# Kernel optimization log

Measured on AMD Instinct MI355X. Metric: run time of the kernel, lower is better.

Reference implementation:

```python
import jax, jax.numpy as jnp
import numpy as np

B, N, C, H = 8, 784, 768, 16
HEAD_DIM = C // H
SCALE = HEAD_DIM ** -0.5


def rel_indices(num_patches):
    # ConViT relative position features: (dx, dy, dx^2+dy^2) per patch pair
    s = int(num_patches ** 0.5)
    ind = (jnp.arange(s)[None, :] - jnp.arange(s)[:, None]).astype(jnp.float32)
    indx = jnp.tile(ind, (s, s))                               # [N, N]
    indy = jnp.repeat(jnp.repeat(ind, s, axis=0), s, axis=1)   # [N, N]
    indd = indx ** 2 + indy ** 2
    return jnp.stack([indx, indy, indd], axis=-1)              # [N, N, 3]


def setup_inputs() -> dict:
    key = jax.random.key(0)
    ks = jax.random.split(key, 6)
    std = 0.02
    return {
        "x": jax.random.normal(ks[0], (B, N, C), dtype=jnp.float32),
        "Wq": jax.random.normal(ks[1], (C, C), dtype=jnp.float32) * std,
        "Wk": jax.random.normal(ks[2], (C, C), dtype=jnp.float32) * std,
        "Wv": jax.random.normal(ks[3], (C, C), dtype=jnp.float32) * std,
        "Wproj": jax.random.normal(ks[4], (C, C), dtype=jnp.float32) * std,
        "b_proj": jnp.zeros((C,), dtype=jnp.float32),
        "W_pos": jax.random.normal(ks[5], (H, 3), dtype=jnp.float32) * std,
        "b_pos": jnp.zeros((H,), dtype=jnp.float32),
        "gating": jnp.ones((H,), dtype=jnp.float32),
    }


def reference(x, Wq, Wk, Wv, Wproj, b_proj, W_pos, b_pos, gating):
    b, n, c = x.shape
    h, d = H, c // H

    def heads(W):
        # torch Linear: y = x @ W.T ; reshape to [b, h, n, d]
        return (x @ W.T).reshape(b, n, h, d).transpose(0, 2, 1, 3)

    q, k, v = heads(Wq), heads(Wk), heads(Wv)

    # content score: [b, h, n, n]
    patch_score = jnp.einsum('bhnd,bhmd->bhnm', q, k) * SCALE
    patch_score = jax.nn.softmax(patch_score, axis=-1)

    # positional score: rel [n,n,3] -> [h,n,n], broadcast over batch
    rel = rel_indices(n)
    pos_score = jnp.einsum('nmc,hc->hnm', rel, W_pos) + b_pos[:, None, None]
    pos_score = jax.nn.softmax(pos_score, axis=-1)

    g = jax.nn.sigmoid(gating)[None, :, None, None]  # [1,h,1,1]
    attn = (1.0 - g) * patch_score + g * pos_score[None]
    attn = attn / jnp.sum(attn, axis=-1, keepdims=True)

    out = jnp.einsum('bhnm,bhmd->bhnd', attn, v)
    out = out.transpose(0, 2, 1, 3).reshape(b, n, c)
    out = out @ Wproj.T + b_proj
    return out, attn, v
```

## Files before the change

### kernel.cpp

```cpp
#include <hip/hip_runtime.h>
#include <math.h>

#define BB 8
#define NN 784
#define CC 768
#define HH 16
#define DD 48
#define SCALE 0.14433756729740643f

#define ATTN_OFF ((size_t)BB*NN*CC)
#define V_OFF (ATTN_OFF + (size_t)BB*HH*NN*NN)

#define WS_XB ((size_t)0)
#define WS_WB ((size_t)4816896)
#define WS_QB (WS_WB + (size_t)4*589824)
#define WS_KB (WS_QB + (size_t)4816896)
#define WS_VT (WS_KB + (size_t)4816896)
#define WS_OB (WS_VT + (size_t)4816896)

using bf16x8 = __attribute__((ext_vector_type(8))) short;
using f32x4  = __attribute__((ext_vector_type(4))) float;

__device__ __forceinline__ short f2bf(float f) {
    union { float f; unsigned u; } uf; uf.f = f;
    unsigned u = uf.u;
    return (short)((u + 0x7FFFu + ((u >> 16) & 1u)) >> 16);
}
__device__ __forceinline__ bf16x8 bzero() {
    bf16x8 z = {0,0,0,0,0,0,0,0};
    return z;
}
__device__ __forceinline__ bf16x8 cvt8v(f32x4 a, f32x4 b) {
    bf16x8 r;
    r[0]=f2bf(a[0]); r[1]=f2bf(a[1]); r[2]=f2bf(a[2]); r[3]=f2bf(a[3]);
    r[4]=f2bf(b[0]); r[5]=f2bf(b[1]); r[6]=f2bf(b[2]); r[7]=f2bf(b[3]);
    return r;
}
#define MFMA16(a,b,c) __builtin_amdgcn_mfma_f32_16x16x32_bf16((a),(b),(c),0,0,0)

__global__ __launch_bounds__(256) void cast_kernel(
    const float* __restrict__ x, const float* __restrict__ Wq,
    const float* __restrict__ Wk, const float* __restrict__ Wv,
    const float* __restrict__ Wp, short* __restrict__ xb, short* __restrict__ wb)
{
    int idx = blockIdx.x * 256 + threadIdx.x;
    const float* src;
    short* dst;
    if (idx < 1204224) {
        src = x + (size_t)idx * 4;
        dst = xb + (size_t)idx * 4;
    } else {
        int j = idx - 1204224;
        int sel = j / 147456;
        size_t off = (size_t)(j % 147456) * 4;
        const float* W = (sel == 0) ? Wq : (sel == 1) ? Wk : (sel == 2) ? Wv : Wp;
        src = W + off;
        dst = wb + (size_t)sel * 589824 + off;
    }
    f32x4 v = *(const f32x4*)src;
    union { short s[4]; uint2 u; } o;
    o.s[0] = f2bf(v[0]); o.s[1] = f2bf(v[1]); o.s[2] = f2bf(v[2]); o.s[3] = f2bf(v[3]);
    *(uint2*)dst = o.u;
}

__global__ __launch_bounds__(256) void qkv_mfma(
    const short* __restrict__ xb, const short* __restrict__ wb,
    short* __restrict__ qb, short* __restrict__ kb,
    float* __restrict__ vo, short* __restrict__ vt)
{
    const int t = threadIdx.x, l = t & 63, ww = t >> 6;
    const int quad = l >> 4, lc = l & 15;
    const int P = blockIdx.x, xcd = P & 7, ii = P >> 3;
    const int start = (xcd < 2) ? xcd * 111 : 222 + (xcd - 2) * 110;
    const int orig = start + ii;
    const int bx = orig / 18, bn = orig % 18;

    const int m0 = bx * 128 + (ww >> 1) * 64;
    const int wsel = bn / 6;
    const int colbase = (bn % 6) * 128 + (ww & 1) * 64;
    const short* W = wb + (size_t)wsel * 589824;

    f32x4 acc[4][4] = {};
    const short* arow = xb + (size_t)(m0 + lc) * 768 + quad * 8;
    const short* brow = W  + (size_t)(colbase + lc) * 768 + quad * 8;

    for (int k0 = 0; k0 < 768; k0 += 32) {
        bf16x8 af[4], bf[4];
#pragma unroll
        for (int i = 0; i < 4; i++) af[i] = *(const bf16x8*)(arow + (size_t)i * 16 * 768 + k0);
#pragma unroll
        for (int j = 0; j < 4; j++) bf[j] = *(const bf16x8*)(brow + (size_t)j * 16 * 768 + k0);
#pragma unroll
        for (int i = 0; i < 4; i++)
#pragma unroll
            for (int j = 0; j < 4; j++)
                acc[i][j] = MFMA16(af[i], bf[j], acc[i][j]);
    }

#pragma unroll
    for (int i = 0; i < 4; i++) {
#pragma unroll
        for (int j = 0; j < 4; j++) {
            const int o = colbase + j * 16 + lc;
            const int h = o / DD, d = o % DD;
#pragma unroll
            for (int r = 0; r < 4; r++) {
                const int m = m0 + i * 16 + quad * 4 + r;
                const int b = m / NN, n = m % NN;
                const size_t bhnd = (((size_t)b * HH + h) * NN + n) * DD + d;
                const float v = acc[i][j][r];
                if (wsel == 0)      qb[bhnd] = f2bf(v);
                else if (wsel == 1) kb[bhnd] = f2bf(v);
                else {
                    __builtin_nontemporal_store(v, vo + bhnd);
                    vt[((size_t)(b * HH + h) * DD + d) * NN + n] = f2bf(v);
                }
            }
        }
    }
}

__global__ __launch_bounds__(256) void attn_pv_fused(
    const short* __restrict__ qb, const short* __restrict__ kb,
    const short* __restrict__ vt,
    const float* __restrict__ W_pos, const float* __restrict__ b_pos,
    const float* __restrict__ gating, float* __restrict__ attn,
    short* __restrict__ ob)
{
    const int t = threadIdx.x, l = t & 63, ww = t >> 6;
    const int quad = l >> 4, lc = l & 15;
    const int P = blockIdx.x;
    const int orig = (P & 7) * 784 + (P >> 3);
    const int bh = orig / 49, b = bh >> 4, h = bh & 15;
    const int row0 = (orig % 49) * 16;

    __shared__ __align__(16) float Sbuf[16][812];
    __shared__ float lxs[55], lys[55], fxs[55], fys[55];
    __shared__ float pmws[16][4];

    Sbuf[t >> 4][784 + (t & 15)] = 0.f;

    const short* qrow = qb + ((size_t)bh * NN + row0 + lc) * DD;
    bf16x8 qf0 = *(const bf16x8*)(qrow + quad * 8);
    bf16x8 qf1 = (quad < 2) ? *(const bf16x8*)(qrow + 32 + quad * 8) : bzero();

    float pmax[4] = {-3e38f, -3e38f, -3e38f, -3e38f};
    {
        int ct = ww;
        const short* krow = kb + ((size_t)bh * NN + ct * 16 + lc) * DD;
        bf16x8 kf0 = *(const bf16x8*)(krow + quad * 8);
        bf16x8 kf1 = (quad < 2) ? *(const bf16x8*)(krow + 32 + quad * 8) : bzero();
        while (ct < 49) {
            const int nct = ct + 4;
            bf16x8 nk0 = bzero(), nk1 = bzero();
            if (nct < 49) {
                const short* nrow = kb + ((size_t)bh * NN + nct * 16 + lc) * DD;
                nk0 = *(const bf16x8*)(nrow + quad * 8);
                nk1 = (quad < 2) ? *(const bf16x8*)(nrow + 32 + quad * 8) : bzero();
            }
            f32x4 cc = {0.f, 0.f, 0.f, 0.f};
            cc = MFMA16(qf0, kf0, cc);
            cc = MFMA16(qf1, kf1, cc);
            const int c0 = ct * 16;
#pragma unroll
            for (int r = 0; r < 4; r++) {
                Sbuf[quad * 4 + r][c0 + lc] = cc[r] * SCALE;
                pmax[r] = fmaxf(pmax[r], cc[r]);
            }
            kf0 = nk0; kf1 = nk1; ct = nct;
        }
    }
#pragma unroll
    for (int r = 0; r < 4; r++) {
        float v = pmax[r];
        v = fmaxf(v, __shfl_xor(v, 1));
        v = fmaxf(v, __shfl_xor(v, 2));
        v = fmaxf(v, __shfl_xor(v, 4));
        v = fmaxf(v, __shfl_xor(v, 8));
        if (lc == 0) pmws[quad * 4 + r][ww] = v;
    }

    const float w0 = W_pos[h * 3], w1 = W_pos[h * 3 + 1], w2 = W_pos[h * 3 + 2];
    if (t < 55) {
        const float d = (float)(t - 27);
        lxs[t] = fmaf(w2, d * d, w0 * d);
    } else if (t >= 64 && t < 119) {
        const float d = (float)(t - 91);
        lys[t - 64] = fmaf(w2, d * d, w1 * d);
    }

    __syncthreads();

    if (t < 55) {
        float m = lxs[0];
#pragma unroll
        for (int i = 1; i < 55; i++) m = fmaxf(m, lxs[i]);
        fxs[t] = __expf(lxs[t] - m);
    } else if (t >= 64 && t < 119) {
        float m = lys[0];
#pragma unroll
        for (int i = 1; i < 55; i++) m = fmaxf(m, lys[i]);
        fys[t - 64] = __expf(lys[t - 64] - m);
    }

    const int r = t >> 4, c = t & 15;
    const int nrow = row0 + r;
    const int nx = nrow % 28, ny = nrow / 28;

    const float sm = SCALE * fmaxf(fmaxf(pmws[r][0], pmws[r][1]),
                                   fmaxf(pmws[r][2], pmws[r][3]));
    float se = 0.f;
#pragma unroll 4
    for (int s = 0; s < 12; s++) {
        f32x4 v = *(const f32x4*)&Sbuf[r][c * 4 + 64 * s];
        v[0] = __expf(v[0] - sm); v[1] = __expf(v[1] - sm);
        v[2] = __expf(v[2] - sm); v[3] = __expf(v[3] - sm);
        *(f32x4*)&Sbuf[r][c * 4 + 64 * s] = v;
        se += (v[0] + v[1]) + (v[2] + v[3]);
    }
    if (c < 4) {
        f32x4 v = *(const f32x4*)&Sbuf[r][768 + c * 4];
        v[0] = __expf(v[0] - sm); v[1] = __expf(v[1] - sm);
        v[2] = __expf(v[2] - sm); v[3] = __expf(v[3] - sm);
        *(f32x4*)&Sbuf[r][768 + c * 4] = v;
        se += (v[0] + v[1]) + (v[2] + v[3]);
    }
    se += __shfl_xor(se, 1);
    se += __shfl_xor(se, 2);
    se += __shfl_xor(se, 4);
    se += __shfl_xor(se, 8);
    const float inv = 1.f / se;
    const float g = 1.f / (1.f + __expf(-gating[h]));

    __syncthreads();

    float Sx = 0.f, Sy = 0.f;
#pragma unroll
    for (int mx = 0; mx < 28; mx++) Sx += fxs[mx - nx + 27];
#pragma unroll
    for (int my = 0; my < 28; my++) Sy += fys[my - ny + 27];
    const float ginv = (1.f - g) * inv;
    const float gp = g / (Sx * Sy);

    float* arow = attn + ((size_t)bh * NN + nrow) * NN;
    const float* fxp = fxs + 27 - nx;
    const float* fyp = fys + 27 - ny;
#define BLEND4(M0)                                                         \
    {                                                                      \
        const int m0_ = (M0);                                              \
        f32x4 v = *(const f32x4*)&Sbuf[r][m0_];                            \
        int mx = m0_ % 28, my = m0_ / 28;                                  \
        f32x4 a;                                                           \
        a[0] = fmaf(v[0], ginv, fxp[mx] * fyp[my] * gp);                   \
        if (++mx == 28) { mx = 0; my++; }                                  \
        a[1] = fmaf(v[1], ginv, fxp[mx] * fyp[my] * gp);                   \
        if (++mx == 28) { mx = 0; my++; }                                  \
        a[2] = fmaf(v[2], ginv, fxp[mx] * fyp[my] * gp);                   \
        if (++mx == 28) { mx = 0; my++; }                                  \
        a[3] = fmaf(v[3], ginv, fxp[mx] * fyp[my] * gp);                   \
        *(f32x4*)&Sbuf[r][m0_] = a;                                        \
        __builtin_nontemporal_store(a, (f32x4*)(arow + m0_));              \
    }
#pragma unroll 4
    for (int s = 0; s < 12; s++) BLEND4(c * 4 + 64 * s);
    if (c < 4) BLEND4(768 + c * 4);
#undef BLEND4

    __syncthreads();

    const short* vbase = vt + (size_t)bh * DD * NN;
    f32x4 acc[3] = {};
    {
        const int kt0 = ww * 6;
        const int kt1 = (ww == 3) ? 25 : kt0 + 6;
        for (int kt = kt0; kt < kt1; kt++) {
            const int k0 = kt * 32 + quad * 8;
            f32x4 a0 = *(const f32x4*)&Sbuf[lc][k0];
            f32x4 a1 = *(const f32x4*)&Sbuf[lc][k0 + 4];
            bf16x8 af = cvt8v(a0, a1);
#pragma unroll
            for (int j = 0; j < 3; j++) {
                bf16x8 bf = (k0 < NN)
                    ? *(const bf16x8*)(vbase + (size_t)(j * 16 + lc) * NN + k0)
                    : bzero();
                acc[j] = MFMA16(af, bf, acc[j]);
            }
        }
    }

    __syncthreads();

    float* Pacc = &Sbuf[0][0];
    if (ww > 0) {
#pragma unroll
        for (int j = 0; j < 3; j++)
            *(f32x4*)&Pacc[(((ww - 1) * 3 + j) * 64 + l) * 4] = acc[j];
    }

    __syncthreads();

    if (ww == 0) {
#pragma unroll
        for (int j = 0; j < 3; j++) {
#pragma unroll
            for (int w = 0; w < 3; w++)
                acc[j] += *(const f32x4*)&Pacc[((w * 3 + j) * 64 + l) * 4];
            const int d = h * DD + j * 16 + lc;
#pragma unroll
            for (int rr = 0; rr < 4; rr++) {
                const int rowi = row0 + quad * 4 + rr;
                ob[((size_t)b * NN + rowi) * CC + d] = f2bf(acc[j][rr]);
            }
        }
    }
}

__global__ __launch_bounds__(256) void proj_mfma(
    const short* __restrict__ ob, const short* __restrict__ wb,
    const float* __restrict__ bias, float* __restrict__ out)
{
    const int t = threadIdx.x, l = t & 63, ww = t >> 6;
    const int quad = l >> 4, lc = l & 15;
    const int P = blockIdx.x, xcd = P & 7, ii = P >> 3;
    const int start = (xcd < 6) ? xcd * 37 : 222 + (xcd - 6) * 36;
    const int orig = start + ii;
    const int bx = orig / 6, by = orig % 6;

    const int m0 = bx * 128 + (ww >> 1) * 64;
    const int colbase = by * 128 + (ww & 1) * 64;
    const short* W = wb + (size_t)3 * 589824;

    f32x4 acc[4][4] = {};
    const short* arow = ob + (size_t)(m0 + lc) * 768 + quad * 8;
    const short* brow = W  + (size_t)(colbase + lc) * 768 + quad * 8;

    for (int k0 = 0; k0 < 768; k0 += 32) {
        bf16x8 af[4], bf[4];
#pragma unroll
        for (int i = 0; i < 4; i++) af[i] = *(const bf16x8*)(arow + (size_t)i * 16 * 768 + k0);
#pragma unroll
        for (int j = 0; j < 4; j++) bf[j] = *(const bf16x8*)(brow + (size_t)j * 16 * 768 + k0);
#pragma unroll
        for (int i = 0; i < 4; i++)
#pragma unroll
            for (int j = 0; j < 4; j++)
                acc[i][j] = MFMA16(af[i], bf[j], acc[i][j]);
    }

#pragma unroll
    for (int i = 0; i < 4; i++) {
#pragma unroll
        for (int j = 0; j < 4; j++) {
            const int o = colbase + j * 16 + lc;
            const float bo = bias[o];
#pragma unroll
            for (int r = 0; r < 4; r++) {
                const int m = m0 + i * 16 + quad * 4 + r;
                __builtin_nontemporal_store(acc[i][j][r] + bo, out + (size_t)m * CC + o);
            }
        }
    }
}

extern "C" void kernel_launch(void* const* d_in, const int* in_sizes, int n_in,
                              void* d_out, int out_size, void* d_ws, size_t ws_size,
                              hipStream_t stream)
{
    const float* x      = (const float*)d_in[0];
    const float* Wq     = (const float*)d_in[1];
    const float* Wk     = (const float*)d_in[2];
    const float* Wv     = (const float*)d_in[3];
    const float* Wproj  = (const float*)d_in[4];
    const float* b_proj = (const float*)d_in[5];
    const float* W_pos  = (const float*)d_in[6];
    const float* b_pos  = (const float*)d_in[7];
    const float* gating = (const float*)d_in[8];

    float* out  = (float*)d_out;
    short* ws   = (short*)d_ws;

    short* xb = ws + WS_XB;
    short* wb = ws + WS_WB;
    short* qb = ws + WS_QB;
    short* kb = ws + WS_KB;
    short* vt = ws + WS_VT;
    short* ob = ws + WS_OB;
    float* attn = out + ATTN_OFF;
    float* vout = out + V_OFF;

    hipLaunchKernelGGL(cast_kernel, dim3(7008), dim3(256), 0, stream,
                       x, Wq, Wk, Wv, Wproj, xb, wb);
    hipLaunchKernelGGL(qkv_mfma, dim3(882), dim3(256), 0, stream,
                       xb, wb, qb, kb, vout, vt);
    hipLaunchKernelGGL(attn_pv_fused, dim3(6272), dim3(256), 0, stream,
                       qb, kb, vt, W_pos, b_pos, gating, attn, ob);
    hipLaunchKernelGGL(proj_mfma, dim3(294), dim3(256), 0, stream,
                       ob, wb, b_proj, out);
}
```

Before: 629.0 us.

## Keep QK scores in registers, fuse exp into score pass, precompute positional tables

The attention kernel now holds the QK^T tile results in registers and applies the exponential directly when writing to shared memory. This removes the separate shared-memory pass that re-read scores to exponentiate them, and the row sums are reduced via shuffles plus a small shared table. The positional softmax max is computed analytically, and the per-row normalisation sums are precomputed once per block by wave 0, replacing per-thread loops. The final PV reduction is spread across three waves instead of one, and launch bounds request 3 blocks per CU, which may raise register pressure given the 13-entry accumulator array.

```diff
diff --git a/kernel.cpp b/kernel.cpp
--- a/kernel.cpp
+++ b/kernel.cpp
@@ -120,7 +120,7 @@
     }
 }
 
-__global__ __launch_bounds__(256) void attn_pv_fused(
+__global__ __launch_bounds__(256, 3) void attn_pv_fused(
     const short* __restrict__ qb, const short* __restrict__ kb,
     const short* __restrict__ vt,
     const float* __restrict__ W_pos, const float* __restrict__ b_pos,
@@ -135,39 +135,70 @@
     const int row0 = (orig % 49) * 16;
 
     __shared__ __align__(16) float Sbuf[16][812];
-    __shared__ float lxs[55], lys[55], fxs[55], fys[55];
-    __shared__ float pmws[16][4];
+    __shared__ float fxs[55], fys[55];
+    __shared__ float Sxs[28], Sys[28], rowfac[16];
+    __shared__ float pmws[16][4], sums[16][4];
 
     Sbuf[t >> 4][784 + (t & 15)] = 0.f;
+
+    if (ww == 0) {
+        const float w0 = W_pos[h * 3], w1 = W_pos[h * 3 + 1], w2 = W_pos[h * 3 + 2];
+        float mx_ = fmaf(fabsf(w0), 27.f, w2 * 729.f);
+        float my_ = fmaf(fabsf(w1), 27.f, w2 * 729.f);
+        if (w2 < 0.f) {
+            mx_ = fmaxf(mx_, -w0 * w0 / (4.f * w2));
+            my_ = fmaxf(my_, -w1 * w1 / (4.f * w2));
+        }
+        if (l < 55) {
+            const float d = (float)(l - 27);
+            fxs[l] = __expf(fmaf(w2, d * d, w0 * d) - mx_);
+            fys[l] = __expf(fmaf(w2, d * d, w1 * d) - my_);
+        }
+        if (l < 56) {
+            const int n_ = (l < 28) ? l : l - 28;
+            const float* tab = (l < 28) ? fxs : fys;
+            float s = 0.f;
+#pragma unroll
+            for (int m = 0; m < 28; m++) s += tab[m - n_ + 27];
+            if (l < 28) Sxs[n_] = s; else Sys[n_] = s;
+        }
+        if (l < 16) {
+            const int nr = row0 + l;
+            rowfac[l] = 1.f / (Sxs[nr % 28] * Sys[nr / 28]);
+        }
+    }
 
     const short* qrow = qb + ((size_t)bh * NN + row0 + lc) * DD;
     bf16x8 qf0 = *(const bf16x8*)(qrow + quad * 8);
     bf16x8 qf1 = (quad < 2) ? *(const bf16x8*)(qrow + 32 + quad * 8) : bzero();
 
+    const short* kbh = kb + (size_t)bh * NN * DD;
+    f32x4 cc[13];
     float pmax[4] = {-3e38f, -3e38f, -3e38f, -3e38f};
     {
-        int ct = ww;
-        const short* krow = kb + ((size_t)bh * NN + ct * 16 + lc) * DD;
-        bf16x8 kf0 = *(const bf16x8*)(krow + quad * 8);
-        bf16x8 kf1 = (quad < 2) ? *(const bf16x8*)(krow + 32 + quad * 8) : bzero();
-        while (ct < 49) {
-            const int nct = ct + 4;
-            bf16x8 nk0 = bzero(), nk1 = bzero();
-            if (nct < 49) {
-                const short* nrow = kb + ((size_t)bh * NN + nct * 16 + lc) * DD;
-                nk0 = *(const bf16x8*)(nrow + quad * 8);
-                nk1 = (quad < 2) ? *(const bf16x8*)(nrow + 32 + quad * 8) : bzero();
+        bf16x8 kc0, kc1, kn0 = bzero(), kn1 = bzero();
+        {
+            const short* kr = kbh + (size_t)(ww * 16 + lc) * DD;
+            kc0 = *(const bf16x8*)(kr + quad * 8);
+            kc1 = (quad < 2) ? *(const bf16x8*)(kr + 32 + quad * 8) : bzero();
+        }
+#pragma unroll
+        for (int i = 0; i < 13; i++) {
+            const int ct = ww + 4 * i;
+            if (ct < 49) {
+                if (ct + 4 < 49) {
+                    const short* kr = kbh + (size_t)((ct + 4) * 16 + lc) * DD;
+                    kn0 = *(const bf16x8*)(kr + quad * 8);
+                    kn1 = (quad < 2) ? *(const bf16x8*)(kr + 32 + quad * 8) : bzero();
+                }
+                f32x4 a = {0.f, 0.f, 0.f, 0.f};
+                a = MFMA16(qf0, kc0, a);
+                a = MFMA16(qf1, kc1, a);
+                cc[i] = a;
+#pragma unroll
+                for (int r = 0; r < 4; r++) pmax[r] = fmaxf(pmax[r], a[r]);
+                kc0 = kn0; kc1 = kn1;
             }
-            f32x4 cc = {0.f, 0.f, 0.f, 0.f};
-            cc = MFMA16(qf0, kf0, cc);
-            cc = MFMA16(qf1, kf1, cc);
-            const int c0 = ct * 16;
-#pragma unroll
-            for (int r = 0; r < 4; r++) {
-                Sbuf[quad * 4 + r][c0 + lc] = cc[r] * SCALE;
-                pmax[r] = fmaxf(pmax[r], cc[r]);
-            }
-            kf0 = nk0; kf1 = nk1; ct = nct;
         }
     }
 #pragma unroll
@@ -180,75 +211,53 @@
         if (lc == 0) pmws[quad * 4 + r][ww] = v;
     }
 
-    const float w0 = W_pos[h * 3], w1 = W_pos[h * 3 + 1], w2 = W_pos[h * 3 + 2];
-    if (t < 55) {
-        const float d = (float)(t - 27);
-        lxs[t] = fmaf(w2, d * d, w0 * d);
-    } else if (t >= 64 && t < 119) {
-        const float d = (float)(t - 91);
-        lys[t - 64] = fmaf(w2, d * d, w1 * d);
-    }
-
     __syncthreads();
 
-    if (t < 55) {
-        float m = lxs[0];
-#pragma unroll
-        for (int i = 1; i < 55; i++) m = fmaxf(m, lxs[i]);
-        fxs[t] = __expf(lxs[t] - m);
-    } else if (t >= 64 && t < 119) {
-        float m = lys[0];
-#pragma unroll
-        for (int i = 1; i < 55; i++) m = fmaxf(m, lys[i]);
-        fys[t - 64] = __expf(lys[t - 64] - m);
-    }
-
-    const int r = t >> 4, c = t & 15;
-    const int nrow = row0 + r;
+    float sm4[4], ps[4];
+#pragma unroll
+    for (int r = 0; r < 4; r++) {
+        sm4[r] = SCALE * fmaxf(fmaxf(pmws[quad * 4 + r][0], pmws[quad * 4 + r][1]),
+                               fmaxf(pmws[quad * 4 + r][2], pmws[quad * 4 + r][3]));
+        ps[r] = 0.f;
+    }
+#pragma unroll
+    for (int i = 0; i < 13; i++) {
+        const int ct = ww + 4 * i;
+        if (ct < 49) {
+#pragma unroll
+            for (int r = 0; r < 4; r++) {
+                const float e = __expf(fmaf(cc[i][r], SCALE, -sm4[r]));
+                ps[r] += e;
+                Sbuf[quad * 4 + r][ct * 16 + lc] = e;
+            }
+        }
+    }
+#pragma unroll
+    for (int r = 0; r < 4; r++) {
+        float v = ps[r];
+        v += __shfl_xor(v, 1);
+        v += __shfl_xor(v, 2);
+        v += __shfl_xor(v, 4);
+        v += __shfl_xor(v, 8);
+        if (lc == 0) sums[quad * 4 + r][ww] = v;
+    }
+
+    __syncthreads();
+
+    const int r_ = t >> 4, c_ = t & 15;
+    const int nrow = row0 + r_;
+    const float g = 1.f / (1.f + __expf(-gating[h]));
+    const float inv = 1.f / ((sums[r_][0] + sums[r_][1]) + (sums[r_][2] + sums[r_][3]));
+    const float ginv = (1.f - g) * inv;
+    const float gp = g * rowfac[r_];
     const int nx = nrow % 28, ny = nrow / 28;
-
-    const float sm = SCALE * fmaxf(fmaxf(pmws[r][0], pmws[r][1]),
-                                   fmaxf(pmws[r][2], pmws[r][3]));
-    float se = 0.f;
-#pragma unroll 4
-    for (int s = 0; s < 12; s++) {
-        f32x4 v = *(const f32x4*)&Sbuf[r][c * 4 + 64 * s];
-        v[0] = __expf(v[0] - sm); v[1] = __expf(v[1] - sm);
-        v[2] = __expf(v[2] - sm); v[3] = __expf(v[3] - sm);
-        *(f32x4*)&Sbuf[r][c * 4 + 64 * s] = v;
-        se += (v[0] + v[1]) + (v[2] + v[3]);
-    }
-    if (c < 4) {
-        f32x4 v = *(const f32x4*)&Sbuf[r][768 + c * 4];
-        v[0] = __expf(v[0] - sm); v[1] = __expf(v[1] - sm);
-        v[2] = __expf(v[2] - sm); v[3] = __expf(v[3] - sm);
-        *(f32x4*)&Sbuf[r][768 + c * 4] = v;
-        se += (v[0] + v[1]) + (v[2] + v[3]);
-    }
-    se += __shfl_xor(se, 1);
-    se += __shfl_xor(se, 2);
-    se += __shfl_xor(se, 4);
-    se += __shfl_xor(se, 8);
-    const float inv = 1.f / se;
-    const float g = 1.f / (1.f + __expf(-gating[h]));
-
-    __syncthreads();
-
-    float Sx = 0.f, Sy = 0.f;
-#pragma unroll
-    for (int mx = 0; mx < 28; mx++) Sx += fxs[mx - nx + 27];
-#pragma unroll
-    for (int my = 0; my < 28; my++) Sy += fys[my - ny + 27];
-    const float ginv = (1.f - g) * inv;
-    const float gp = g / (Sx * Sy);
-
-    float* arow = attn + ((size_t)bh * NN + nrow) * NN;
     const float* fxp = fxs + 27 - nx;
     const float* fyp = fys + 27 - ny;
+    float* arow = attn + ((size_t)bh * NN + nrow) * NN;
 #define BLEND4(M0)                                                         \
     {                                                                      \
         const int m0_ = (M0);                                              \
-        f32x4 v = *(const f32x4*)&Sbuf[r][m0_];                            \
+        f32x4 v = *(const f32x4*)&Sbuf[r_][m0_];                           \
         int mx = m0_ % 28, my = m0_ / 28;                                  \
         f32x4 a;                                                           \
         a[0] = fmaf(v[0], ginv, fxp[mx] * fyp[my] * gp);                   \
@@ -258,12 +267,12 @@
         a[2] = fmaf(v[2], ginv, fxp[mx] * fyp[my] * gp);                   \
         if (++mx == 28) { mx = 0; my++; }                                  \
         a[3] = fmaf(v[3], ginv, fxp[mx] * fyp[my] * gp);                   \
-        *(f32x4*)&Sbuf[r][m0_] = a;                                        \
+        *(f32x4*)&Sbuf[r_][m0_] = a;                                       \
         __builtin_nontemporal_store(a, (f32x4*)(arow + m0_));              \
     }
 #pragma unroll 4
-    for (int s = 0; s < 12; s++) BLEND4(c * 4 + 64 * s);
-    if (c < 4) BLEND4(768 + c * 4);
+    for (int s = 0; s < 12; s++) BLEND4(c_ * 4 + 64 * s);
+    if (c_ < 4) BLEND4(768 + c_ * 4);
 #undef BLEND4
 
     __syncthreads();
@@ -291,27 +300,21 @@
     __syncthreads();
 
     float* Pacc = &Sbuf[0][0];
-    if (ww > 0) {
-#pragma unroll
-        for (int j = 0; j < 3; j++)
-            *(f32x4*)&Pacc[(((ww - 1) * 3 + j) * 64 + l) * 4] = acc[j];
-    }
+#pragma unroll
+    for (int j = 0; j < 3; j++)
+        *(f32x4*)&Pacc[((ww * 3 + j) * 64 + l) * 4] = acc[j];
 
     __syncthreads();
 
-    if (ww == 0) {
-#pragma unroll
-        for (int j = 0; j < 3; j++) {
-#pragma unroll
-            for (int w = 0; w < 3; w++)
-                acc[j] += *(const f32x4*)&Pacc[((w * 3 + j) * 64 + l) * 4];
-            const int d = h * DD + j * 16 + lc;
-#pragma unroll
-            for (int rr = 0; rr < 4; rr++) {
-                const int rowi = row0 + quad * 4 + rr;
-                ob[((size_t)b * NN + rowi) * CC + d] = f2bf(acc[j][rr]);
-            }
-        }
+    if (ww < 3) {
+        f32x4 s = {0.f, 0.f, 0.f, 0.f};
+#pragma unroll
+        for (int w = 0; w < 4; w++)
+            s += *(const f32x4*)&Pacc[((w * 3 + ww) * 64 + l) * 4];
+        const int d = h * DD + ww * 16 + lc;
+#pragma unroll
+        for (int rr = 0; rr < 4; rr++)
+            ob[((size_t)b * NN + row0 + quad * 4 + rr) * CC + d] = f2bf(s[rr]);
     }
 }
 
```

New measurement: 621.1 us. About the same (-1.2%).
